# Performance work log

Measured on AMD Instinct MI355X. Metric: run time of the kernel, lower is better.

Reference implementation:

```python
import jax, jax.numpy as jnp
import numpy as np

B, L, H = 2, 2048, 1024
NH = 4
K = int(H * 0.5)       # key_dim = 512
V = int(H * 1.0)       # value_dim = 1024
DK, DV = K // NH, V // NH   # 128, 256
PR = 32                # proj_low_rank_dim
GR = 64                # gate_low_rank_dim
EPS = 1e-5


def setup_inputs() -> dict:
    key = jax.random.key(0)
    ks = jax.random.split(key, 16)
    s = 0.02
    return {
        "x": jax.random.normal(ks[0], (B, L, H), jnp.float32),
        "mu_x": jax.random.normal(ks[1], (H,), jnp.float32) * s,      # LerpLinear mu of x_proj[0]
        "Wx1": jax.random.normal(ks[2], (5 * PR, H), jnp.float32) * s,  # x_proj[0].linear
        "Wx2": jax.random.normal(ks[3], (H, 5 * PR), jnp.float32) * s,  # x_proj[2]
        "x_bias": jax.random.normal(ks[4], (5, H), jnp.float32) * s,
        "Wr": jax.random.normal(ks[5], (K, H), jnp.float32) * s,
        "Wk": jax.random.normal(ks[6], (K, H), jnp.float32) * s,
        "Wv": jax.random.normal(ks[7], (V, H), jnp.float32) * s,
        "Wg": jax.random.normal(ks[8], (V, H), jnp.float32) * s,
        "Ww1": jax.random.normal(ks[9], (GR, H), jnp.float32) * s,     # w_proj LoRA down
        "Ww2": jax.random.normal(ks[10], (K, GR), jnp.float32) * s,    # w_proj LoRA up
        "bw2": jax.random.normal(ks[11], (K,), jnp.float32) * s,
        "bonus": jax.random.normal(ks[12], (NH, DK), jnp.float32) * s,  # u
        "ln_w": jnp.ones((DV,), jnp.float32),
        "ln_b": jnp.zeros((DV,), jnp.float32),
        "Wo": jax.random.normal(ks[13], (H, V), jnp.float32) * s,
    }


def reference(x, mu_x, Wx1, Wx2, x_bias, Wr, Wk, Wv, Wg, Ww1, Ww2, bw2,
              bonus, ln_w, ln_b, Wo):
    b, l, h = x.shape
    # token shift: shifted[t] = x[t-1], zeros at t=0 (nn.ZeroPad2d((0,0,1,-1)))
    shifted = jnp.pad(x, ((0, 0), (1, 0), (0, 0)))[:, :-1]
    delta = shifted - x

    # x_proj: LerpLinear -> tanh -> einsum with o_proj-like weight, 5 mixing vectors
    xp = jnp.tanh((x + delta * mu_x) @ Wx1.T).reshape(b, l, 5, PR)
    mus = jnp.einsum('blnr,hnr->blnh', xp, Wx2.reshape(H, 5, PR)) + x_bias
    mu_r, mu_w, mu_k, mu_v, mu_g = (mus[:, :, i] for i in range(5))

    # DDLerpLinear projections: linear(x + delta * mu)
    r = (x + delta * mu_r) @ Wr.T                                   # [B,L,K]
    w = jnp.tanh((x + delta * mu_w) @ Ww1.T) @ Ww2.T + bw2          # LoRA, [B,L,K]
    k = (x + delta * mu_k) @ Wk.T                                   # [B,L,K]
    v = (x + delta * mu_v) @ Wv.T                                   # [B,L,V]
    g = (x + delta * mu_g) @ Wg.T                                   # [B,L,V]

    r = r.reshape(b, l, NH, DK)
    k = k.reshape(b, l, NH, DK)
    v = v.reshape(b, l, NH, DV)
    w = -jnp.exp(w.reshape(b, l, NH, DK))   # log-decay (negative)

    def step(S, inp):
        r_t, k_t, v_t, w_t = inp                                    # [B,h,dk]/[B,h,dv]
        kv = k_t[..., :, None] * v_t[..., None, :]                  # [B,h,dk,dv]
        o_t = jnp.einsum('bhk,bhkv->bhv', r_t,
                         S + bonus[None, :, :, None] * kv)
        S = jnp.exp(w_t)[..., None] * S + kv
        return S, o_t

    seq = (r.transpose(1, 0, 2, 3), k.transpose(1, 0, 2, 3),
           v.transpose(1, 0, 2, 3), w.transpose(1, 0, 2, 3))
    S0 = jnp.zeros((b, NH, DK, DV), x.dtype)
    _, o = jax.lax.scan(step, S0, seq)       # [L,B,h,dv]
    o = o.transpose(1, 0, 2, 3)              # [B,L,h,dv]

    # per-head LayerNorm fused with swish gate
    mean = o.mean(-1, keepdims=True)
    var = o.var(-1, keepdims=True)
    o = (o - mean) * jax.lax.rsqrt(var + EPS) * ln_w + ln_b
    gh = g.reshape(b, l, NH, DV)
    o = o * (gh * jax.nn.sigmoid(gh))        # swish gate

    return o.reshape(b, l, V) @ Wo.T         # [B,L,H]
```

## Files before the change

### kernel.cpp

```cpp
#include <hip/hip_runtime.h>
#include <cstdint>
#include <cstddef>

#define H     1024
#define LSEQ  2048
#define NHH   4
#define DKK   128
#define DVV   256
#define KDIM  512
#define VDIM  1024
#define GRR   64
#define MTOT  4096
#define SEGL  128
#define NSEG  16

enum { EPI_NONE = 0, EPI_TANH = 1, EPI_DEC = 3 };

typedef __attribute__((ext_vector_type(8))) _Float16 half8;
typedef __attribute__((ext_vector_type(4))) float f32x4;
typedef __attribute__((ext_vector_type(2))) float f32x2;

static __device__ __forceinline__ unsigned short f2h(float f) {
    _Float16 h = (_Float16)f;
    union { _Float16 h; unsigned short u; } c;
    c.h = h;
    return c.u;
}

template<int CTRL>
static __device__ __forceinline__ float dpp_add(float x) {
    int xi = __float_as_int(x);
    int mv = __builtin_amdgcn_update_dpp(0, xi, CTRL, 0xf, 0xf, true);
    return x + __int_as_float(mv);
}

__global__ __launch_bounds__(256) void lerp5_kernel(
    const float* __restrict__ xp,
    const float* __restrict__ Wx2,
    const float* __restrict__ xb,
    const float* __restrict__ x,
    unsigned short* __restrict__ insb)
{
    __shared__ float As[16][64];
    __shared__ float Bs[16][64];
    const int m0 = blockIdx.x * 64;
    const int n0 = blockIdx.y * 64;
    const int t  = threadIdx.x;
    const int tx = t & 15, ty = t >> 4;
    const int sm = t >> 2;
    const int sq = (t & 3) * 4;
    const int nbase = n0 + tx * 4;

    float4 xv[4], pv[4];
#pragma unroll
    for (int i = 0; i < 4; i++) {
        const int m = m0 + ty * 4 + i;
        xv[i] = *(const float4*)(x + (size_t)m * H + nbase);
        pv[i] = make_float4(0.f, 0.f, 0.f, 0.f);
        if ((m & (LSEQ - 1)) != 0)
            pv[i] = *(const float4*)(x + (size_t)(m - 1) * H + nbase);
    }

    for (int z = 0; z < 5; z++) {
        const int acol = z * 32;
        float acc[4][4];
#pragma unroll
        for (int i = 0; i < 4; i++)
#pragma unroll
            for (int j = 0; j < 4; j++) acc[i][j] = 0.f;

#pragma unroll
        for (int k0 = 0; k0 < 32; k0 += 16) {
            {
                const int m = m0 + sm;
                const float4 av = *(const float4*)(xp + (size_t)m * 256 + acol + k0 + sq);
                As[sq + 0][sm] = av.x; As[sq + 1][sm] = av.y;
                As[sq + 2][sm] = av.z; As[sq + 3][sm] = av.w;
            }
            {
                const int n = n0 + sm;
                const float4 bv = *(const float4*)(Wx2 + (size_t)n * 160 + acol + k0 + sq);
                Bs[sq + 0][sm] = bv.x; Bs[sq + 1][sm] = bv.y;
                Bs[sq + 2][sm] = bv.z; Bs[sq + 3][sm] = bv.w;
            }
            __syncthreads();
#pragma unroll
            for (int kk = 0; kk < 16; kk++) {
                const float4 a = *(const float4*)&As[kk][ty * 4];
                const float4 b = *(const float4*)&Bs[kk][tx * 4];
                const float av2[4] = {a.x, a.y, a.z, a.w};
                const float bv2[4] = {b.x, b.y, b.z, b.w};
#pragma unroll
                for (int i = 0; i < 4; i++)
#pragma unroll
                    for (int j = 0; j < 4; j++) acc[i][j] += av2[i] * bv2[j];
            }
            __syncthreads();
        }

        const float4 bb = *(const float4*)(xb + z * H + nbase);
        unsigned short* dst = insb + (size_t)z * 4194304;
#pragma unroll
        for (int i = 0; i < 4; i++) {
            const int m = m0 + ty * 4 + i;
            float4 r;
            r.x = xv[i].x + (pv[i].x - xv[i].x) * (acc[i][0] + bb.x);
            r.y = xv[i].y + (pv[i].y - xv[i].y) * (acc[i][1] + bb.y);
            r.z = xv[i].z + (pv[i].z - xv[i].z) * (acc[i][2] + bb.z);
            r.w = xv[i].w + (pv[i].w - xv[i].w) * (acc[i][3] + bb.w);
            ushort4 p;
            p.x = f2h(r.x); p.y = f2h(r.y); p.z = f2h(r.z); p.w = f2h(r.w);
            *(ushort4*)(dst + (size_t)m * H + nbase) = p;
        }
    }
}

template<int EPI>
__global__ __launch_bounds__(256) void gemm_mfma_bt(
    const unsigned short* __restrict__ A,
    const unsigned short* __restrict__ A2, int nsplit, int lda,
    const unsigned short* __restrict__ B, int ldb,
    float* __restrict__ C, unsigned short* __restrict__ Ch, int ldc, int K,
    const float* __restrict__ bias)
{
    __shared__ __align__(16) unsigned short As[128 * 32];
    __shared__ __align__(16) unsigned short Bs[128 * 32];
    const int t    = threadIdx.x;
    const int w    = t >> 6;
    const int lane = t & 63;
    const int m0 = blockIdx.x * 128;
    const int n0 = blockIdx.y * 128;
    const unsigned short* Au = (n0 < nsplit) ? A : A2;
    const int mw = (w & 1) * 64;
    const int nw = (w >> 1) * 64;
    const int l15 = lane & 15;
    const int q4  = lane >> 4;

    f32x4 acc[4][4];
#pragma unroll
    for (int i = 0; i < 4; i++)
#pragma unroll
        for (int j = 0; j < 4; j++) {
            f32x4 z = {0.f, 0.f, 0.f, 0.f};
            acc[i][j] = z;
        }

    for (int k0 = 0; k0 < K; k0 += 32) {
        __syncthreads();
#pragma unroll
        for (int jj = 0; jj < 2; jj++) {
            const int c   = w * 128 + jj * 64 + lane;
            const int row = c >> 2;
            const int col = (c & 3) * 8;
            __builtin_amdgcn_global_load_lds(
                (const __attribute__((address_space(1))) void*)(Au + (size_t)(m0 + row) * lda + k0 + col),
                (__attribute__((address_space(3))) void*)((char*)As + (w * 128 + jj * 64) * 16),
                16, 0, 0);
            __builtin_amdgcn_global_load_lds(
                (const __attribute__((address_space(1))) void*)(B + (size_t)(n0 + row) * ldb + k0 + col),
                (__attribute__((address_space(3))) void*)((char*)Bs + (w * 128 + jj * 64) * 16),
                16, 0, 0);
        }
        __syncthreads();

        half8 a[4], b[4];
#pragma unroll
        for (int i = 0; i < 4; i++)
            a[i] = *(const half8*)(As + (mw + i * 16 + l15) * 32 + q4 * 8);
#pragma unroll
        for (int j = 0; j < 4; j++)
            b[j] = *(const half8*)(Bs + (nw + j * 16 + l15) * 32 + q4 * 8);
#pragma unroll
        for (int i = 0; i < 4; i++)
#pragma unroll
            for (int j = 0; j < 4; j++)
                acc[i][j] = __builtin_amdgcn_mfma_f32_16x16x32_f16(a[i], b[j], acc[i][j], 0, 0, 0);
    }

#pragma unroll
    for (int i = 0; i < 4; i++) {
        const int m_base = m0 + mw + i * 16 + q4 * 4;
#pragma unroll
        for (int j = 0; j < 4; j++) {
            const int n = n0 + nw + j * 16 + l15;
#pragma unroll
            for (int r = 0; r < 4; r++) {
                float val = acc[i][j][r];
                if constexpr (EPI == EPI_TANH) {
                    C[(size_t)(m_base + r) * ldc + n] = tanhf(val);
                } else if constexpr (EPI == EPI_DEC) {
                    C[(size_t)(m_base + r) * ldc + n] = expf(-expf(val + bias[n]));
                } else {
                    C[(size_t)(m_base + r) * ldc + n] = val;
                }
            }
        }
    }
}

__global__ __launch_bounds__(256) void gemm_fused3(
    const unsigned short* __restrict__ s0, const unsigned short* __restrict__ s1,
    const unsigned short* __restrict__ s2, const unsigned short* __restrict__ s3,
    const unsigned short* __restrict__ s4,
    const unsigned short* __restrict__ Ww1p, const unsigned short* __restrict__ Wrb,
    const unsigned short* __restrict__ Wvb,
    unsigned short* __restrict__ wlow16, float* __restrict__ rkB,
    float* __restrict__ vgB)
{
    const int y = blockIdx.y;
    const unsigned short *Au, *Bp;
    float* C = nullptr;
    unsigned short* Ch = nullptr;
    int n0, ldc;
    if (y == 0) {
        Au = s1; Bp = Ww1p; n0 = 0; ldc = 128; Ch = wlow16;
    } else if (y <= 8) {
        n0 = (y - 1) * 128;
        Au = (n0 < 512) ? s0 : s2;
        Bp = Wrb; C = rkB; ldc = 1024;
    } else {
        n0 = (y - 9) * 128;
        Au = (n0 < 1024) ? s3 : s4;
        Bp = Wvb; C = vgB; ldc = 2048;
    }

    __shared__ __align__(16) unsigned short As[128 * 32];
    __shared__ __align__(16) unsigned short Bs[128 * 32];
    const int t    = threadIdx.x;
    const int w    = t >> 6;
    const int lane = t & 63;
    const int m0 = blockIdx.x * 128;
    const int mw = (w & 1) * 64;
    const int nw = (w >> 1) * 64;
    const int l15 = lane & 15;
    const int q4  = lane >> 4;

    f32x4 acc[4][4];
#pragma unroll
    for (int i = 0; i < 4; i++)
#pragma unroll
        for (int j = 0; j < 4; j++) {
            f32x4 z = {0.f, 0.f, 0.f, 0.f};
            acc[i][j] = z;
        }

    for (int k0 = 0; k0 < H; k0 += 32) {
        __syncthreads();
#pragma unroll
        for (int jj = 0; jj < 2; jj++) {
            const int c   = w * 128 + jj * 64 + lane;
            const int row = c >> 2;
            const int col = (c & 3) * 8;
            __builtin_amdgcn_global_load_lds(
                (const __attribute__((address_space(1))) void*)(Au + (size_t)(m0 + row) * H + k0 + col),
                (__attribute__((address_space(3))) void*)((char*)As + (w * 128 + jj * 64) * 16),
                16, 0, 0);
            __builtin_amdgcn_global_load_lds(
                (const __attribute__((address_space(1))) void*)(Bp + (size_t)(n0 + row) * H + k0 + col),
                (__attribute__((address_space(3))) void*)((char*)Bs + (w * 128 + jj * 64) * 16),
                16, 0, 0);
        }
        __syncthreads();

        half8 a[4], b[4];
#pragma unroll
        for (int i = 0; i < 4; i++)
            a[i] = *(const half8*)(As + (mw + i * 16 + l15) * 32 + q4 * 8);
#pragma unroll
        for (int j = 0; j < 4; j++)
            b[j] = *(const half8*)(Bs + (nw + j * 16 + l15) * 32 + q4 * 8);
#pragma unroll
        for (int i = 0; i < 4; i++)
#pragma unroll
            for (int j = 0; j < 4; j++)
                acc[i][j] = __builtin_amdgcn_mfma_f32_16x16x32_f16(a[i], b[j], acc[i][j], 0, 0, 0);
    }

#pragma unroll
    for (int i = 0; i < 4; i++) {
        const int m_base = m0 + mw + i * 16 + q4 * 4;
#pragma unroll
        for (int j = 0; j < 4; j++) {
            const int n = n0 + nw + j * 16 + l15;
#pragma unroll
            for (int r = 0; r < 4; r++) {
                float val = acc[i][j][r];
                if (Ch) Ch[(size_t)(m_base + r) * ldc + n] = f2h(tanhf(val));
                else    C[(size_t)(m_base + r) * ldc + n] = val;
            }
        }
    }
}

__global__ __launch_bounds__(256) void gemm_mfma_corr(
    const unsigned short* __restrict__ rt16,
    const unsigned short* __restrict__ SentryT16,
    float* __restrict__ o)
{
    const int z   = blockIdx.z;
    const int seg = (z >> 3) + 1;
    const int bh  = z & 7;
    const int b   = bh >> 2, h = bh & 3;
    const unsigned short* A = rt16 + ((size_t)b * LSEQ + seg * SEGL) * KDIM + h * DKK;
    const unsigned short* B = SentryT16 + (size_t)(seg * 8 + bh) * 32768;
    float* C = o + ((size_t)b * LSEQ + seg * SEGL) * VDIM + h * DVV;

    __shared__ __align__(16) unsigned short As[128 * 32];
    __shared__ __align__(16) unsigned short Bs[128 * 32];
    const int t    = threadIdx.x;
    const int w    = t >> 6;
    const int lane = t & 63;
    const int m0 = blockIdx.x * 128;
    const int n0 = blockIdx.y * 128;
    const int mw = (w & 1) * 64;
    const int nw = (w >> 1) * 64;
    const int l15 = lane & 15;
    const int q4  = lane >> 4;

    f32x4 acc[4][4];
#pragma unroll
    for (int i = 0; i < 4; i++)
#pragma unroll
        for (int j = 0; j < 4; j++) {
            f32x4 zz = {0.f, 0.f, 0.f, 0.f};
            acc[i][j] = zz;
        }

    for (int k0 = 0; k0 < 128; k0 += 32) {
        __syncthreads();
#pragma unroll
        for (int jj = 0; jj < 2; jj++) {
            const int c   = w * 128 + jj * 64 + lane;
            const int row = c >> 2;
            const int col = (c & 3) * 8;
            __builtin_amdgcn_global_load_lds(
                (const __attribute__((address_space(1))) void*)(A + (size_t)(m0 + row) * KDIM + k0 + col),
                (__attribute__((address_space(3))) void*)((char*)As + (w * 128 + jj * 64) * 16),
                16, 0, 0);
            __builtin_amdgcn_global_load_lds(
                (const __attribute__((address_space(1))) void*)(B + (size_t)(n0 + row) * 128 + k0 + col),
                (__attribute__((address_space(3))) void*)((char*)Bs + (w * 128 + jj * 64) * 16),
                16, 0, 0);
        }
        __syncthreads();

        half8 a[4], bb[4];
#pragma unroll
        for (int i = 0; i < 4; i++)
            a[i] = *(const half8*)(As + (mw + i * 16 + l15) * 32 + q4 * 8);
#pragma unroll
        for (int j = 0; j < 4; j++)
            bb[j] = *(const half8*)(Bs + (nw + j * 16 + l15) * 32 + q4 * 8);
#pragma unroll
        for (int i = 0; i < 4; i++)
#pragma unroll
            for (int j = 0; j < 4; j++)
                acc[i][j] = __builtin_amdgcn_mfma_f32_16x16x32_f16(a[i], bb[j], acc[i][j], 0, 0, 0);
    }

#pragma unroll
    for (int i = 0; i < 4; i++) {
        const int m_base = m0 + mw + i * 16 + q4 * 4;
#pragma unroll
        for (int j = 0; j < 4; j++) {
            const int n = n0 + nw + j * 16 + l15;
#pragma unroll
            for (int rr = 0; rr < 4; rr++)
                C[(size_t)(m_base + rr) * VDIM + n] += acc[i][j][rr];
        }
    }
}

__global__ __launch_bounds__(256) void prep_kernel(
    const float* __restrict__ Wr, const float* __restrict__ Wk,
    const float* __restrict__ Wv, const float* __restrict__ Wg,
    const float* __restrict__ Wo, const float* __restrict__ Wx1,
    const float* __restrict__ Ww1, const float* __restrict__ Ww2,
    unsigned short* __restrict__ Wb, unsigned short* __restrict__ Wx1p,
    unsigned short* __restrict__ Ww1p, unsigned short* __restrict__ Ww2p,
    const float* __restrict__ x, const float* __restrict__ mux,
    unsigned short* __restrict__ xl16)
{
    const int bx = blockIdx.x;
    if (bx < 4512) {
        const int q = bx * 256 + threadIdx.x;
        float4 v = make_float4(0.f, 0.f, 0.f, 0.f);
        unsigned short* dst;
        if (q < 1048576) {
            const int i4 = q * 4;
            const float* src; int off;
            if      (i4 <  524288) { src = Wr; off = i4; }
            else if (i4 < 1048576) { src = Wk; off = i4 -  524288; }
            else if (i4 < 2097152) { src = Wv; off = i4 - 1048576; }
            else if (i4 < 3145728) { src = Wg; off = i4 - 2097152; }
            else                   { src = Wo; off = i4 - 3145728; }
            v = *(const float4*)(src + off);
            dst = Wb + i4;
        } else if (q < 1114112) {
            const int e = (q - 1048576) * 4;
            const int row = e >> 10;
            if (row < 160) v = *(const float4*)(Wx1 + (size_t)row * H + (e & 1023));
            dst = Wx1p + e;
        } else if (q < 1146880) {
            const int e = (q - 1114112) * 4;
            const int row = e >> 10;
            if (row < 64) v = *(const float4*)(Ww1 + (size_t)row * H + (e & 1023));
            dst = Ww1p + e;
        } else {
            const int e = (q - 1146880) * 4;
            v = *(const float4*)(Ww2 + e);
            dst = Ww2p + e;
        }
        ushort4 o4;
        o4.x = f2h(v.x); o4.y = f2h(v.y); o4.z = f2h(v.z); o4.w = f2h(v.w);
        *(ushort4*)dst = o4;
    } else {
        const int m = bx - 4512;
        const int c = threadIdx.x * 4;
        const float4 xv = *(const float4*)(x + (size_t)m * H + c);
        float4 pv = make_float4(0.f, 0.f, 0.f, 0.f);
        if ((m & (LSEQ - 1)) != 0)
            pv = *(const float4*)(x + (size_t)(m - 1) * H + c);
        const float4 mv = *(const float4*)(mux + c);
        ushort4 p;
        p.x = f2h(xv.x + (pv.x - xv.x) * mv.x);
        p.y = f2h(xv.y + (pv.y - xv.y) * mv.y);
        p.z = f2h(xv.z + (pv.z - xv.z) * mv.z);
        p.w = f2h(xv.w + (pv.w - xv.w) * mv.w);
        *(ushort4*)(xl16 + (size_t)m * H + c) = p;
    }
}

__global__ __launch_bounds__(256, 4) void scan_pass1(
    const float* __restrict__ rk, const float* __restrict__ vg,
    const float* __restrict__ dec, const float* __restrict__ bonus,
    float* __restrict__ o, unsigned short* __restrict__ rt16,
    float* __restrict__ Sloc, float* __restrict__ Dtot)
{
    const int bh  = blockIdx.x & 7;
    const int vc  = (blockIdx.x >> 3) & 7;
    const int seg = blockIdx.x >> 6;
    const int b   = bh >> 2;
    const int h   = bh & 3;
    const int t   = threadIdx.x;
    const int kg  = t & 31;
    const int vl  = t >> 5;
    const bool wlead = (vc == 0) && (vl == 0);

    f32x2 S2[4][2];
    float D[4] = {1.f, 1.f, 1.f, 1.f}, u[4];
#pragma unroll
    for (int j = 0; j < 4; j++) {
        u[j] = bonus[h * DKK + kg * 4 + j];
        f32x2 z = {0.f, 0.f};
        S2[j][0] = z; S2[j][1] = z;
    }

    const size_t row0 = (size_t)b * LSEQ + (size_t)seg * SEGL;
    const float* rp = rk  + row0 * 1024 + h * DKK + kg * 4;
    const float* dp = dec + row0 * 512  + h * DKK + kg * 4;
    const float* vp = vg  + row0 * 2048 + h * DVV + vc * 32 + vl * 4;
    float*       op = o   + row0 * 1024 + h * DVV + vc * 32 + vl * 4;
    unsigned short* rt = rt16 + row0 * 512 + h * DKK + kg * 4;

    float4 cr = *(const float4*)rp;
    float4 ck = *(const float4*)(rp + 512);
    float4 cd = *(const float4*)dp;
    float4 cv = *(const float4*)vp;
    rp += 1024; dp += 512; vp += 2048;

#pragma unroll 2
    for (int t0 = 0; t0 < SEGL; ++t0) {
        const float4 nr = *(const float4*)rp;
        const float4 nk = *(const float4*)(rp + 512);
        const float4 nd = *(const float4*)dp;
        const float4 nv = *(const float4*)vp;
        rp += 1024; dp += 512; vp += 2048;

        if (wlead) {
            ushort4 p;
            p.x = f2h(cr.x * D[0]); p.y = f2h(cr.y * D[1]);
            p.z = f2h(cr.z * D[2]); p.w = f2h(cr.w * D[3]);
            *(ushort4*)rt = p;
        }
        rt += 512;

        const float ra[4] = {cr.x, cr.y, cr.z, cr.w};
        const float ka[4] = {ck.x, ck.y, ck.z, ck.w};
        const float da[4] = {cd.x, cd.y, cd.z, cd.w};
        f32x2 va2[2];
        va2[0].x = cv.x; va2[0].y = cv.y;
        va2[1].x = cv.z; va2[1].y = cv.w;
        f32x2 part2[2];
        part2[0] = (f32x2){0.f, 0.f};
        part2[1] = (f32x2){0.f, 0.f};
#pragma unroll
        for (int j = 0; j < 4; j++) {
#pragma unroll
            for (int p = 0; p < 2; p++) {
                const f32x2 kv2 = va2[p] * ka[j];
                part2[p] += ra[j] * (S2[j][p] + u[j] * kv2);
                S2[j][p] = da[j] * S2[j][p] + kv2;
            }
            D[j] *= da[j];
        }
        float part[4] = {part2[0].x, part2[0].y, part2[1].x, part2[1].y};
#pragma unroll
        for (int jj = 0; jj < 4; jj++) {
            part[jj] = dpp_add<0xB1>(part[jj]);
            part[jj] = dpp_add<0x4E>(part[jj]);
            part[jj] = dpp_add<0x141>(part[jj]);
            part[jj] = dpp_add<0x140>(part[jj]);
            part[jj] = dpp_add<0x142>(part[jj]);
        }
        if (kg == 31) {
            float4 res = make_float4(part[0], part[1], part[2], part[3]);
            *(float4*)op = res;
        }
        op += 1024;
        cr = nr; ck = nk; cd = nd; cv = nv;
    }

    {
        float* sl = Sloc + (size_t)(seg * 8 + bh) * 32768
                    + (size_t)(kg * 4) * 256 + vc * 32 + vl * 4;
#pragma unroll
        for (int j = 0; j < 4; j++) {
            float4 sv = make_float4(S2[j][0].x, S2[j][0].y, S2[j][1].x, S2[j][1].y);
            *(float4*)(sl + j * 256) = sv;
        }
        if (wlead) {
            float* dt = Dtot + (seg * 8 + bh) * 128 + kg * 4;
#pragma unroll
            for (int j = 0; j < 4; j++) dt[j] = D[j];
        }
    }
}

__global__ __launch_bounds__(256) void scan_pass2(
    const float* __restrict__ Sloc, const float* __restrict__ Dtot,
    unsigned short* __restrict__ SentryT16)
{
    const int vc = blockIdx.x & 31;
    const int bh = blockIdx.x >> 5;
    const int t  = threadIdx.x;
    const int kg = t & 31;
    const int vl = t >> 5;

    float S[4] = {0.f, 0.f, 0.f, 0.f};
    for (int p = 0; p < NSEG; p++) {
        unsigned short* st = SentryT16 + (size_t)(p * 8 + bh) * 32768
                             + (size_t)(vc * 8 + vl) * 128 + kg * 4;
        ushort4 pk;
        pk.x = f2h(S[0]); pk.y = f2h(S[1]); pk.z = f2h(S[2]); pk.w = f2h(S[3]);
        *(ushort4*)st = pk;
        if (p < NSEG - 1) {
            const float* sl = Sloc + (size_t)(p * 8 + bh) * 32768
                              + (size_t)(kg * 4) * 256 + vc * 8 + vl;
            const float* dt = Dtot + (p * 8 + bh) * 128 + kg * 4;
#pragma unroll
            for (int j = 0; j < 4; j++) S[j] = dt[j] * S[j] + sl[j * 256];
        }
    }
}

__global__ __launch_bounds__(256) void ln_gate_kernel(
    const float* __restrict__ o, const float* __restrict__ vg,
    const float* __restrict__ lnw, const float* __restrict__ lnb,
    unsigned short* __restrict__ out)
{
    const int m    = blockIdx.x;
    const int t    = threadIdx.x;
    const int h    = t >> 6;
    const int lane = t & 63;
    const size_t obase = (size_t)m * VDIM + (size_t)h * DVV + lane * 4;
    const size_t gbase = (size_t)m * 2048 + 1024 + (size_t)h * DVV + lane * 4;
    const float4 ov = *(const float4*)(o + obase);
    float sum = ov.x + ov.y + ov.z + ov.w;
    float sq  = ov.x * ov.x + ov.y * ov.y + ov.z * ov.z + ov.w * ov.w;
#pragma unroll
    for (int off = 1; off < 64; off <<= 1) {
        sum += __shfl_xor(sum, off);
        sq  += __shfl_xor(sq, off);
    }
    const float mean = sum * (1.f / DVV);
    const float var  = sq * (1.f / DVV) - mean * mean;
    const float rstd = rsqrtf(var + 1e-5f);
    const float4 gv = *(const float4*)(vg + gbase);
    const float4 wv = *(const float4*)(lnw + lane * 4);
    const float4 bv = *(const float4*)(lnb + lane * 4);
    float4 res;
    res.x = ((ov.x - mean) * rstd * wv.x + bv.x) * (gv.x / (1.f + expf(-gv.x)));
    res.y = ((ov.y - mean) * rstd * wv.y + bv.y) * (gv.y / (1.f + expf(-gv.y)));
    res.z = ((ov.z - mean) * rstd * wv.z + bv.z) * (gv.z / (1.f + expf(-gv.z)));
    res.w = ((ov.w - mean) * rstd * wv.w + bv.w) * (gv.w / (1.f + expf(-gv.w)));
    ushort4 p;
    p.x = f2h(res.x); p.y = f2h(res.y); p.z = f2h(res.z); p.w = f2h(res.w);
    *(ushort4*)(out + obase) = p;
}

extern "C" void kernel_launch(void* const* d_in, const int* in_sizes, int n_in,
                              void* d_out, int out_size, void* d_ws, size_t ws_size,
                              hipStream_t stream)
{
    const float* x     = (const float*)d_in[0];
    const float* mu_x  = (const float*)d_in[1];
    const float* Wx1   = (const float*)d_in[2];
    const float* Wx2   = (const float*)d_in[3];
    const float* xb    = (const float*)d_in[4];
    const float* Wr    = (const float*)d_in[5];
    const float* Wk    = (const float*)d_in[6];
    const float* Wv    = (const float*)d_in[7];
    const float* Wg    = (const float*)d_in[8];
    const float* Ww1   = (const float*)d_in[9];
    const float* Ww2   = (const float*)d_in[10];
    const float* bw2   = (const float*)d_in[11];
    const float* bonus = (const float*)d_in[12];
    const float* lnw   = (const float*)d_in[13];
    const float* lnb   = (const float*)d_in[14];
    const float* Wo    = (const float*)d_in[15];
    float* out = (float*)d_out;
    (void)in_sizes; (void)n_in; (void)out_size; (void)ws_size;

    float* ws = (float*)d_ws;
    unsigned short* Wx1p = (unsigned short*)(ws + 0);
    unsigned short* Ww1p = (unsigned short*)(ws + 131072);
    unsigned short* Ww2p = (unsigned short*)(ws + 196608);
    unsigned short* Wb   = (unsigned short*)(ws + 212992);
    float* xp     = ws + 2310144;
    unsigned short* wlow16 = (unsigned short*)(ws + 3358720);
    float* insB   = ws + 3620864;
    float* rkB    = ws + 14106624;
    float* vgB    = ws + 18301952;
    float* decB   = ws + 26692608;

    unsigned short* insb = (unsigned short*)insB;
    unsigned short* Wrb  = Wb;
    unsigned short* Wvb  = Wb + 1048576;
    unsigned short* Wob  = Wb + 3145728;
    unsigned short* xl16 = (unsigned short*)rkB;
    float*          o       = insB;
    unsigned short* rt16    = insb + 2ul * 4194304;
    float*          Sloc    = insB + 3ul * 2097152;
    float*          Dtot    = (float*)wlow16;
    unsigned short* SentryT16 = (unsigned short*)decB;
    unsigned short* gatedb  = (unsigned short*)(insB + 3ul * 2097152);

    dim3 blk(256);

    prep_kernel<<<dim3(8608), blk, 0, stream>>>(Wr, Wk, Wv, Wg, Wo, Wx1, Ww1, Ww2,
                                                Wb, Wx1p, Ww1p, Ww2p, x, mu_x, xl16);

    gemm_mfma_bt<EPI_TANH><<<dim3(32, 2), blk, 0, stream>>>(
        xl16, xl16, 1 << 30, H, Wx1p, H, xp, nullptr, 256, H, nullptr);

    lerp5_kernel<<<dim3(64, 16), blk, 0, stream>>>(xp, Wx2, xb, x, insb);

    gemm_fused3<<<dim3(32, 25), blk, 0, stream>>>(
        insb + 0ul * 4194304, insb + 1ul * 4194304, insb + 2ul * 4194304,
        insb + 3ul * 4194304, insb + 4ul * 4194304,
        Ww1p, Wrb, Wvb, wlow16, rkB, vgB);

    gemm_mfma_bt<EPI_DEC><<<dim3(32, 4), blk, 0, stream>>>(
        wlow16, wlow16, 1 << 30, 128, Ww2p, 64, decB, nullptr, KDIM, 64, bw2);

    scan_pass1<<<dim3(1024), blk, 0, stream>>>(rkB, vgB, decB, bonus, o, rt16, Sloc, Dtot);
    scan_pass2<<<dim3(256), blk, 0, stream>>>(Sloc, Dtot, SentryT16);
    gemm_mfma_corr<<<dim3(1, 2, 120), blk, 0, stream>>>(rt16, SentryT16, o);

    ln_gate_kernel<<<dim3(4096), blk, 0, stream>>>(o, vgB, lnw, lnb, gatedb);

    gemm_mfma_bt<EPI_NONE><<<dim3(32, 8), blk, 0, stream>>>(
        gatedb, gatedb, 1 << 30, VDIM, Wob, VDIM, out, nullptr, H, VDIM, nullptr);
}
```

Before: 386.5 us.

## Split chunked scan into 32 segments when workspace allows, raise scan occupancy

The scan is now split into 32 segments of 64 steps instead of 16 of 128 when the workspace is large enough. This doubles the blocks in the sequential pass-1 scan and halves each block's serial chain, at the cost of a longer pass-2 carry chain and more correction GEMM blocks. Because the correction GEMM still uses 128-row tiles, its stores are masked to the segment length, and its Sloc/Sentry buffers move to new workspace offsets. Launch bounds go from 4 to 8 blocks per CU and the DPP reductions now work on float pairs, with the added register pressure risking spills.

```diff
diff --git a/kernel.cpp b/kernel.cpp
--- a/kernel.cpp
+++ b/kernel.cpp
@@ -11,8 +11,6 @@
 #define VDIM  1024
 #define GRR   64
 #define MTOT  4096
-#define SEGL  128
-#define NSEG  16
 
 enum { EPI_NONE = 0, EPI_TANH = 1, EPI_DEC = 3 };
 
@@ -28,10 +26,13 @@
 }
 
 template<int CTRL>
-static __device__ __forceinline__ float dpp_add(float x) {
-    int xi = __float_as_int(x);
-    int mv = __builtin_amdgcn_update_dpp(0, xi, CTRL, 0xf, 0xf, true);
-    return x + __int_as_float(mv);
+static __device__ __forceinline__ f32x2 dpp_add2(f32x2 x) {
+    int lo = __builtin_amdgcn_update_dpp(0, __float_as_int(x.x), CTRL, 0xf, 0xf, true);
+    int hi = __builtin_amdgcn_update_dpp(0, __float_as_int(x.y), CTRL, 0xf, 0xf, true);
+    f32x2 m;
+    m.x = __int_as_float(lo);
+    m.y = __int_as_float(hi);
+    return x + m;
 }
 
 __global__ __launch_bounds__(256) void lerp5_kernel(
@@ -295,15 +296,15 @@
 __global__ __launch_bounds__(256) void gemm_mfma_corr(
     const unsigned short* __restrict__ rt16,
     const unsigned short* __restrict__ SentryT16,
-    float* __restrict__ o)
+    float* __restrict__ o, int segl)
 {
     const int z   = blockIdx.z;
     const int seg = (z >> 3) + 1;
     const int bh  = z & 7;
     const int b   = bh >> 2, h = bh & 3;
-    const unsigned short* A = rt16 + ((size_t)b * LSEQ + seg * SEGL) * KDIM + h * DKK;
+    const unsigned short* A = rt16 + ((size_t)b * LSEQ + (size_t)seg * segl) * KDIM + h * DKK;
     const unsigned short* B = SentryT16 + (size_t)(seg * 8 + bh) * 32768;
-    float* C = o + ((size_t)b * LSEQ + seg * SEGL) * VDIM + h * DVV;
+    float* C = o + ((size_t)b * LSEQ + (size_t)seg * segl) * VDIM + h * DVV;
 
     __shared__ __align__(16) unsigned short As[128 * 32];
     __shared__ __align__(16) unsigned short Bs[128 * 32];
@@ -360,13 +361,15 @@
 
 #pragma unroll
     for (int i = 0; i < 4; i++) {
-        const int m_base = m0 + mw + i * 16 + q4 * 4;
+        const int mrow = mw + i * 16 + q4 * 4;
+        const int m_base = m0 + mrow;
 #pragma unroll
         for (int j = 0; j < 4; j++) {
             const int n = n0 + nw + j * 16 + l15;
 #pragma unroll
             for (int rr = 0; rr < 4; rr++)
-                C[(size_t)(m_base + rr) * VDIM + n] += acc[i][j][rr];
+                if (mrow + rr < segl)
+                    C[(size_t)(m_base + rr) * VDIM + n] += acc[i][j][rr];
         }
     }
 }
@@ -431,11 +434,11 @@
     }
 }
 
-__global__ __launch_bounds__(256, 4) void scan_pass1(
+__global__ __launch_bounds__(256, 8) void scan_pass1(
     const float* __restrict__ rk, const float* __restrict__ vg,
     const float* __restrict__ dec, const float* __restrict__ bonus,
     float* __restrict__ o, unsigned short* __restrict__ rt16,
-    float* __restrict__ Sloc, float* __restrict__ Dtot)
+    float* __restrict__ Sloc, float* __restrict__ Dtot, int segl)
 {
     const int bh  = blockIdx.x & 7;
     const int vc  = (blockIdx.x >> 3) & 7;
@@ -456,7 +459,7 @@
         S2[j][0] = z; S2[j][1] = z;
     }
 
-    const size_t row0 = (size_t)b * LSEQ + (size_t)seg * SEGL;
+    const size_t row0 = (size_t)b * LSEQ + (size_t)seg * segl;
     const float* rp = rk  + row0 * 1024 + h * DKK + kg * 4;
     const float* dp = dec + row0 * 512  + h * DKK + kg * 4;
     const float* vp = vg  + row0 * 2048 + h * DVV + vc * 32 + vl * 4;
@@ -470,7 +473,7 @@
     rp += 1024; dp += 512; vp += 2048;
 
 #pragma unroll 2
-    for (int t0 = 0; t0 < SEGL; ++t0) {
+    for (int t0 = 0; t0 < segl; ++t0) {
         const float4 nr = *(const float4*)rp;
         const float4 nk = *(const float4*)(rp + 512);
         const float4 nd = *(const float4*)dp;
@@ -504,17 +507,16 @@
             }
             D[j] *= da[j];
         }
-        float part[4] = {part2[0].x, part2[0].y, part2[1].x, part2[1].y};
-#pragma unroll
-        for (int jj = 0; jj < 4; jj++) {
-            part[jj] = dpp_add<0xB1>(part[jj]);
-            part[jj] = dpp_add<0x4E>(part[jj]);
-            part[jj] = dpp_add<0x141>(part[jj]);
-            part[jj] = dpp_add<0x140>(part[jj]);
-            part[jj] = dpp_add<0x142>(part[jj]);
+#pragma unroll
+        for (int p = 0; p < 2; p++) {
+            part2[p] = dpp_add2<0xB1>(part2[p]);
+            part2[p] = dpp_add2<0x4E>(part2[p]);
+            part2[p] = dpp_add2<0x141>(part2[p]);
+            part2[p] = dpp_add2<0x140>(part2[p]);
+            part2[p] = dpp_add2<0x142>(part2[p]);
         }
         if (kg == 31) {
-            float4 res = make_float4(part[0], part[1], part[2], part[3]);
+            float4 res = make_float4(part2[0].x, part2[0].y, part2[1].x, part2[1].y);
             *(float4*)op = res;
         }
         op += 1024;
@@ -539,7 +541,7 @@
 
 __global__ __launch_bounds__(256) void scan_pass2(
     const float* __restrict__ Sloc, const float* __restrict__ Dtot,
-    unsigned short* __restrict__ SentryT16)
+    unsigned short* __restrict__ SentryT16, int nseg)
 {
     const int vc = blockIdx.x & 31;
     const int bh = blockIdx.x >> 5;
@@ -548,13 +550,13 @@
     const int vl = t >> 5;
 
     float S[4] = {0.f, 0.f, 0.f, 0.f};
-    for (int p = 0; p < NSEG; p++) {
+    for (int p = 0; p < nseg; p++) {
         unsigned short* st = SentryT16 + (size_t)(p * 8 + bh) * 32768
                              + (size_t)(vc * 8 + vl) * 128 + kg * 4;
         ushort4 pk;
         pk.x = f2h(S[0]); pk.y = f2h(S[1]); pk.z = f2h(S[2]); pk.w = f2h(S[3]);
         *(ushort4*)st = pk;
-        if (p < NSEG - 1) {
+        if (p < nseg - 1) {
             const float* sl = Sloc + (size_t)(p * 8 + bh) * 32768
                               + (size_t)(kg * 4) * 256 + vc * 8 + vl;
             const float* dt = Dtot + (p * 8 + bh) * 128 + kg * 4;
@@ -620,7 +622,7 @@
     const float* lnb   = (const float*)d_in[14];
     const float* Wo    = (const float*)d_in[15];
     float* out = (float*)d_out;
-    (void)in_sizes; (void)n_in; (void)out_size; (void)ws_size;
+    (void)in_sizes; (void)n_in; (void)out_size;
 
     float* ws = (float*)d_ws;
     unsigned short* Wx1p = (unsigned short*)(ws + 0);
@@ -641,10 +643,16 @@
     unsigned short* xl16 = (unsigned short*)rkB;
     float*          o       = insB;
     unsigned short* rt16    = insb + 2ul * 4194304;
-    float*          Sloc    = insB + 3ul * 2097152;
     float*          Dtot    = (float*)wlow16;
-    unsigned short* SentryT16 = (unsigned short*)decB;
     unsigned short* gatedb  = (unsigned short*)(insB + 3ul * 2097152);
+
+    const size_t need32 = 41373184ull * sizeof(float);
+    const int  nseg = (ws_size >= need32) ? 32 : 16;
+    const int  segl = LSEQ / nseg;
+    float* Sloc = (nseg == 32) ? (ws + 28790272)
+                               : (insB + 3ul * 2097152);
+    unsigned short* SentryT16 = (nseg == 32) ? (unsigned short*)(ws + 37178880)
+                                             : (unsigned short*)decB;
 
     dim3 blk(256);
 
@@ -664,9 +672,11 @@
     gemm_mfma_bt<EPI_DEC><<<dim3(32, 4), blk, 0, stream>>>(
         wlow16, wlow16, 1 << 30, 128, Ww2p, 64, decB, nullptr, KDIM, 64, bw2);
 
-    scan_pass1<<<dim3(1024), blk, 0, stream>>>(rkB, vgB, decB, bonus, o, rt16, Sloc, Dtot);
-    scan_pass2<<<dim3(256), blk, 0, stream>>>(Sloc, Dtot, SentryT16);
-    gemm_mfma_corr<<<dim3(1, 2, 120), blk, 0, stream>>>(rt16, SentryT16, o);
+    scan_pass1<<<dim3(nseg * 64), blk, 0, stream>>>(rkB, vgB, decB, bonus,
+                                                    o, rt16, Sloc, Dtot, segl);
+    scan_pass2<<<dim3(256), blk, 0, stream>>>(Sloc, Dtot, SentryT16, nseg);
+    gemm_mfma_corr<<<dim3(1, 2, (nseg - 1) * 8), blk, 0, stream>>>(
+        rt16, SentryT16, o, segl);
 
     ln_gate_kernel<<<dim3(4096), blk, 0, stream>>>(o, vgB, lnw, lnb, gatedb);
 
```

Result: slower. 919.0 us (+137.8%).
